# Kernel optimization log

Measured on AMD Instinct MI355X. Metric: run time of the kernel, lower is better.

Reference implementation:

```python
import jax, jax.numpy as jnp
import numpy as np

N = 20000; E = 320000; IN = 128; H = 6; C = 64; HC = H * C; NC = 16; NG = 64


def _gatv2(x, src, dst, wl, bl, wr, br, att, bias, heads, out_c, concat):
    # PyG GATv2Conv (eval mode, share_weights=False, negative_slope=0.2)
    n = x.shape[0]
    xl = (x @ wl + bl).reshape(n, heads, out_c)   # source-side transform
    xr = (x @ wr + br).reshape(n, heads, out_c)   # target-side transform
    # edge-wise attention logits: leaky_relu(x_l[j] + x_r[i]) . att
    e = jnp.einsum('ehc,hc->eh', jax.nn.leaky_relu(xl[src] + xr[dst], 0.2), att)
    # segment softmax over incoming edges of each target node
    emax = jax.ops.segment_max(e, dst, num_segments=n)
    a = jnp.exp(e - emax[dst])
    denom = jax.ops.segment_sum(a, dst, num_segments=n)
    alpha = a / (denom[dst] + 1e-16)
    out = jax.ops.segment_sum(xl[src] * alpha[:, :, None], dst, num_segments=n)
    out = out.reshape(n, heads * out_c) if concat else out.mean(axis=1)
    return out + bias


def setup_inputs() -> dict:
    key = jax.random.key(0)
    ks = jax.random.split(key, 32)
    s = 0.05
    inp = {}
    inp['x'] = jax.random.normal(ks[0], (N, IN), jnp.float32)
    inp['edge_index'] = jax.random.randint(ks[1], (2, E), 0, N, dtype=jnp.int32)
    inp['batch'] = jnp.sort(jax.random.randint(ks[2], (N,), 0, NG, dtype=jnp.int32))
    # input projection (input_dim != hidden_dim * n_heads)
    inp['inp_w'] = jax.random.normal(ks[3], (IN, HC), jnp.float32) * s
    inp['inp_b'] = jnp.zeros((HC,), jnp.float32)
    # layer 0: IN -> (H, C), concat
    inp['l0_wl'] = jax.random.normal(ks[4], (IN, HC), jnp.float32) * s
    inp['l0_bl'] = jnp.zeros((HC,), jnp.float32)
    inp['l0_wr'] = jax.random.normal(ks[5], (IN, HC), jnp.float32) * s
    inp['l0_br'] = jnp.zeros((HC,), jnp.float32)
    inp['l0_att'] = jax.random.normal(ks[6], (H, C), jnp.float32) * s
    inp['l0_bias'] = jnp.zeros((HC,), jnp.float32)
    # layer 1: HC -> (H, C), concat
    inp['l1_wl'] = jax.random.normal(ks[7], (HC, HC), jnp.float32) * s
    inp['l1_bl'] = jnp.zeros((HC,), jnp.float32)
    inp['l1_wr'] = jax.random.normal(ks[8], (HC, HC), jnp.float32) * s
    inp['l1_br'] = jnp.zeros((HC,), jnp.float32)
    inp['l1_att'] = jax.random.normal(ks[9], (H, C), jnp.float32) * s
    inp['l1_bias'] = jnp.zeros((HC,), jnp.float32)
    # layer 2: HC -> (1, C), no concat (mean over the single head)
    inp['l2_wl'] = jax.random.normal(ks[10], (HC, C), jnp.float32) * s
    inp['l2_bl'] = jnp.zeros((C,), jnp.float32)
    inp['l2_wr'] = jax.random.normal(ks[11], (HC, C), jnp.float32) * s
    inp['l2_br'] = jnp.zeros((C,), jnp.float32)
    inp['l2_att'] = jax.random.normal(ks[12], (1, C), jnp.float32) * s
    inp['l2_bias'] = jnp.zeros((C,), jnp.float32)
    # residual projection HC -> C at the last layer (bias-free Linear)
    inp['res_w'] = jax.random.normal(ks[13], (HC, C), jnp.float32) * s
    # dense head: Linear(C,C) + BatchNorm1d(eval) + ReLU + Linear(C,NC)
    inp['d1_w'] = jax.random.normal(ks[14], (C, C), jnp.float32) * s
    inp['d1_b'] = jnp.zeros((C,), jnp.float32)
    inp['bn_g'] = jnp.ones((C,), jnp.float32)
    inp['bn_b'] = jnp.zeros((C,), jnp.float32)
    inp['bn_m'] = jnp.zeros((C,), jnp.float32)
    inp['bn_v'] = jnp.ones((C,), jnp.float32)
    inp['d2_w'] = jax.random.normal(ks[15], (C, NC), jnp.float32) * s
    inp['d2_b'] = jnp.zeros((NC,), jnp.float32)
    return inp


def reference(x, edge_index, batch, inp_w, inp_b,
              l0_wl, l0_bl, l0_wr, l0_br, l0_att, l0_bias,
              l1_wl, l1_bl, l1_wr, l1_br, l1_att, l1_bias,
              l2_wl, l2_bl, l2_wr, l2_br, l2_att, l2_bias,
              res_w, d1_w, d1_b, bn_g, bn_b, bn_m, bn_v, d2_w, d2_b):
    n = x.shape[0]
    sl = jnp.arange(n, dtype=edge_index.dtype)           # self-loops (PyG default)
    src = jnp.concatenate([edge_index[0], sl])
    dst = jnp.concatenate([edge_index[1], sl])
    x_res = x @ inp_w + inp_b
    h = jax.nn.elu(_gatv2(x, src, dst, l0_wl, l0_bl, l0_wr, l0_br, l0_att, l0_bias, H, C, True)) + x_res
    x_res = h
    h = jax.nn.elu(_gatv2(h, src, dst, l1_wl, l1_bl, l1_wr, l1_br, l1_att, l1_bias, H, C, True)) + x_res
    x_res = h
    h = jax.nn.elu(_gatv2(h, src, dst, l2_wl, l2_bl, l2_wr, l2_br, l2_att, l2_bias, 1, C, False)) + x_res @ res_w
    pooled = jax.ops.segment_sum(h, batch, num_segments=NG)
    z = pooled @ d1_w + d1_b
    z = (z - bn_m) / jnp.sqrt(bn_v + 1e-5) * bn_g + bn_b  # BatchNorm1d eval
    z = jax.nn.relu(z) @ d2_w + d2_b
    return h, z
```

## Files before the change

kernel.cpp:

```cpp
#include <hip/hip_runtime.h>
#include <hip/hip_bf16.h>
#include <math.h>

#define NN 20000
#define EE 320000
#define IND 128
#define HH 6
#define CC 64
#define HCC 384
#define NCC 16
#define NGG 64

typedef __bf16 bf16x8 __attribute__((ext_vector_type(8)));
typedef float f32x4 __attribute__((ext_vector_type(4)));
typedef float f32x2 __attribute__((ext_vector_type(2)));
typedef unsigned short ushort_t;
typedef unsigned int uint_t;

#define LOG2E 1.44269504088896f

__device__ inline ushort_t f2bf(float f) {
    union { float f; uint_t u; } x; x.f = f;
    uint_t r = (x.u + 0x7FFF + ((x.u >> 16) & 1)) >> 16;
    return (ushort_t)r;
}
__device__ inline void bf8cvt2(uint4 v, f32x2* f) {
    union { uint_t u; float x; } a, b;
    a.u = v.x << 16; b.u = v.x & 0xFFFF0000u; f[0] = (f32x2){a.x, b.x};
    a.u = v.y << 16; b.u = v.y & 0xFFFF0000u; f[1] = (f32x2){a.x, b.x};
    a.u = v.z << 16; b.u = v.z & 0xFFFF0000u; f[2] = (f32x2){a.x, b.x};
    a.u = v.w << 16; b.u = v.w & 0xFFFF0000u; f[3] = (f32x2){a.x, b.x};
}

template <int CTRL>
__device__ inline float dppadd(float x) {
    int y = __builtin_amdgcn_mov_dpp(__builtin_bit_cast(int, x), CTRL, 0xF, 0xF, true);
    return x + __builtin_bit_cast(float, y);
}

__device__ inline void load_lds16(const ushort_t* g, ushort_t* l) {
    __builtin_amdgcn_global_load_lds(
        (const __attribute__((address_space(1))) void*)g,
        (__attribute__((address_space(3))) void*)l, 16, 0, 0);
}


__global__ void zero_init_kernel(int* counts, int* s6_tail, int* s1_tail, int n) {
    int t = blockIdx.x * blockDim.x + threadIdx.x;
    if (t < n) counts[t] = 0;
    if (t < 8) { s6_tail[t] = 0; s1_tail[t] = 0; }
}

__global__ void count_kernel(const int* __restrict__ ei, int* __restrict__ counts, int E) {
    int t = blockIdx.x * blockDim.x + threadIdx.x;
    if (t < E) atomicAdd(&counts[ei[E + t]], 1);
}

__global__ __launch_bounds__(1024) void scan_kernel(
    const int* __restrict__ counts, int* __restrict__ offsets,
    int* __restrict__ cursor, int n) {
    __shared__ int buf[NN];
    __shared__ int part[1024];
    int t = threadIdx.x;
    for (int idx = t; idx < n; idx += 1024) buf[idx] = counts[idx] + 1;
    __syncthreads();
    int per = (n + 1023) / 1024;
    int base = t * per;
    int sum = 0;
    for (int j = 0; j < per; ++j) {
        int idx = base + j;
        if (idx < n) sum += buf[idx];
    }
    part[t] = sum;
    __syncthreads();
    for (int off = 1; off < 1024; off <<= 1) {
        int v = (t >= off) ? part[t - off] : 0;
        __syncthreads();
        part[t] += v;
        __syncthreads();
    }
    int run = (t == 0) ? 0 : part[t - 1];
    for (int j = 0; j < per; ++j) {
        int idx = base + j;
        if (idx < n) {
            int deg = buf[idx];
            buf[idx] = run;
            run += deg;
        }
    }
    __syncthreads();
    for (int idx = t; idx < n; idx += 1024) {
        int v = buf[idx];
        offsets[idx] = v;
        cursor[idx] = v;
    }
    if (t == 1023) offsets[n] = run;
}

__global__ void fill_kernel(const int* __restrict__ ei, int* __restrict__ cursor,
                            int* __restrict__ srcs6, int* __restrict__ srcs1,
                            int E, int n) {
    int t = blockIdx.x * blockDim.x + threadIdx.x;
    if (t < E) {
        int s = ei[t];
        int d = ei[E + t];
        int slot = atomicAdd(&cursor[d], 1);
        srcs6[slot] = s * 1536;
        srcs1[slot] = s << 8;
    } else if (t < E + n) {
        int i = t - E;
        int slot = atomicAdd(&cursor[i], 1);
        srcs6[slot] = i * 1536;
        srcs1[slot] = i << 8;
    }
}

#define WBIG (1152 * IND)
#define WC1 (768 * HCC)
#define WC2 (192 * HCC)
#define XB_N (NN * IND)
#define PREP_TOTAL (WBIG + WC1 + WC2 + XB_N + 1152 + 768 + 192)

__global__ void prep_kernel(const float* __restrict__ x, const float* __restrict__ inp_w,
    const float* __restrict__ l0wl, const float* __restrict__ l0wr,
    const float* __restrict__ l1wl, const float* __restrict__ l1wr,
    const float* __restrict__ l2wl, const float* __restrict__ l2wr,
    const float* __restrict__ resw,
    const float* __restrict__ inp_b,
    const float* __restrict__ l0bl, const float* __restrict__ l0br,
    const float* __restrict__ l1bl, const float* __restrict__ l1br,
    const float* __restrict__ l2bl, const float* __restrict__ l2br,
    ushort_t* wBig, ushort_t* wC1, ushort_t* wC2, ushort_t* xb,
    float* bBig, float* bC1, float* bC2)
{
    int i = blockIdx.x * blockDim.x + threadIdx.x;
    if (i >= PREP_TOTAL) return;
    if (i < WBIG) {
        int col = i >> 7, k = i & 127;
        float v;
        if (col < 384)      v = inp_w[k * 384 + col];
        else if (col < 768) v = l0wl[k * 384 + (col - 384)];
        else                v = l0wr[k * 384 + (col - 768)];
        wBig[i] = f2bf(v); return;
    }
    i -= WBIG;
    if (i < WC1) {
        int col = i / 384, k = i - col * 384;
        float v = col < 384 ? l1wl[k * 384 + col] : l1wr[k * 384 + (col - 384)];
        wC1[i] = f2bf(v); return;
    }
    i -= WC1;
    if (i < WC2) {
        int col = i / 384, k = i - col * 384;
        float v;
        if (col < 64)       v = resw[k * 64 + col];
        else if (col < 128) v = l2wl[k * 64 + (col - 64)];
        else                v = l2wr[k * 64 + (col - 128)];
        wC2[i] = f2bf(v); return;
    }
    i -= WC2;
    if (i < XB_N) { xb[i] = f2bf(x[i]); return; }
    i -= XB_N;
    if (i < 1152) {
        float v;
        if (i < 384)      v = inp_b[i];
        else if (i < 768) v = l0bl[i - 384];
        else              v = l0br[i - 768];
        bBig[i] = v; return;
    }
    i -= 1152;
    if (i < 768) { bC1[i] = i < 384 ? l1bl[i] : l1br[i - 384]; return; }
    i -= 768;
    if (i < 192) {
        float v;
        if (i < 64)       v = 0.0f;
        else if (i < 128) v = l2bl[i - 64];
        else              v = l2br[i - 128];
        bC2[i] = v; return;
    }
}

__global__ __launch_bounds__(512) void gemm_mfma2(
    const ushort_t* __restrict__ A, const ushort_t* __restrict__ BT,
    const float* __restrict__ bias,
    ushort_t* __restrict__ Cb1, int ld1,
    ushort_t* __restrict__ Cb2, int ld2, int split,
    int M, int N, int K, int NT)
{
    __shared__ ushort_t Bs[2][2][128 * 32];
    int t = threadIdx.x;
    int w = t >> 6, L = t & 63;
    int m0 = blockIdx.x * 256;
    int q = L >> 4, r16 = L & 15;
    int lr = L >> 2;
    int lc = ((L & 3) ^ ((lr >> 1) & 3)) * 8;
    int sw = (q ^ ((r16 >> 1) & 3)) * 8;
    int oB = (w * 16) * 32;

    int rA0 = min(m0 + w * 32 + r16, M - 1);
    int rA1 = min(m0 + w * 32 + 16 + r16, M - 1);
    const ushort_t* pA0base = A + (size_t)rA0 * K + q * 8;
    const ushort_t* pA1base = A + (size_t)rA1 * K + q * 8;

    for (int nt = 0; nt < NT; ++nt) {
        int n0 = (blockIdx.y * NT + nt) * 128;
        int rB = min(n0 + w * 16 + lr, N - 1);
        const ushort_t* gB = BT + (size_t)rB * K + lc;
        const ushort_t* pA0 = pA0base;
        const ushort_t* pA1 = pA1base;

        f32x4 acc[2][8];
#pragma unroll
        for (int a = 0; a < 2; ++a)
#pragma unroll
            for (int b = 0; b < 8; ++b) acc[a][b] = (f32x4){0.f, 0.f, 0.f, 0.f};

        load_lds16(gB, &Bs[0][0][oB]);
        load_lds16(gB + 32, &Bs[0][1][oB]);
        gB += 64;
        bf16x8 a0 = *(const bf16x8*)pA0;
        bf16x8 a2 = *(const bf16x8*)(pA0 + 32);
        bf16x8 a1 = *(const bf16x8*)pA1;
        bf16x8 a3 = *(const bf16x8*)(pA1 + 32);
        pA0 += 64; pA1 += 64;

        int buf = 0;
        for (int k0 = 0; k0 < K; k0 += 64) {
            __syncthreads();
            bool more = (k0 + 64 < K);
            if (more) {
                int nb = buf ^ 1;
                load_lds16(gB, &Bs[nb][0][oB]);
                load_lds16(gB + 32, &Bs[nb][1][oB]);
                gB += 64;
            }
            bf16x8 na0, na1, na2, na3;
            if (more) {
                na0 = *(const bf16x8*)pA0;
                na2 = *(const bf16x8*)(pA0 + 32);
                na1 = *(const bf16x8*)pA1;
                na3 = *(const bf16x8*)(pA1 + 32);
                pA0 += 64; pA1 += 64;
            }
#pragma unroll
            for (int ct = 0; ct < 8; ++ct) {
                bf16x8 blo = *(const bf16x8*)&Bs[buf][0][(ct * 16 + r16) * 32 + sw];
                bf16x8 bhi = *(const bf16x8*)&Bs[buf][1][(ct * 16 + r16) * 32 + sw];
                acc[0][ct] = __builtin_amdgcn_mfma_f32_16x16x32_bf16(blo, a0, acc[0][ct], 0, 0, 0);
                acc[1][ct] = __builtin_amdgcn_mfma_f32_16x16x32_bf16(blo, a1, acc[1][ct], 0, 0, 0);
                acc[0][ct] = __builtin_amdgcn_mfma_f32_16x16x32_bf16(bhi, a2, acc[0][ct], 0, 0, 0);
                acc[1][ct] = __builtin_amdgcn_mfma_f32_16x16x32_bf16(bhi, a3, acc[1][ct], 0, 0, 0);
            }
            if (more) { a0 = na0; a1 = na1; a2 = na2; a3 = na3; }
            buf ^= 1;
        }
#pragma unroll
        for (int rt = 0; rt < 2; ++rt) {
            int row = m0 + w * 32 + rt * 16 + r16;
            if (row >= M) continue;
#pragma unroll
            for (int ct = 0; ct < 8; ++ct) {
                int colb = n0 + ct * 16 + q * 4;
                if (colb >= N) continue;
                float4 bv = *(const float4*)(bias + colb);
                uint2 pk;
                pk.x = (uint_t)f2bf(acc[rt][ct][0] + bv.x) | ((uint_t)f2bf(acc[rt][ct][1] + bv.y) << 16);
                pk.y = (uint_t)f2bf(acc[rt][ct][2] + bv.z) | ((uint_t)f2bf(acc[rt][ct][3] + bv.w) << 16);
                if (colb < split)
                    *(uint2*)(Cb1 + (size_t)row * ld1 + colb) = pk;
                else
                    *(uint2*)(Cb2 + (size_t)row * ld2 + (colb - split)) = pk;
            }
        }
    }
}

__global__ __launch_bounds__(256) void gemm_mfma(
    const ushort_t* __restrict__ A, const ushort_t* __restrict__ BT,
    const float* __restrict__ bias,
    float* __restrict__ Cf, ushort_t* __restrict__ Cb1, int ld1,
    ushort_t* __restrict__ Cb2, int ld2, int split,
    int M, int N, int K)
{
    __shared__ ushort_t Bs[2][2][128 * 32];
    int t = threadIdx.x;
    int w = t >> 6, L = t & 63;
    int m0 = blockIdx.x * 128, n0 = blockIdx.y * 128;
    int q = L >> 4, r16 = L & 15;

    f32x4 acc[2][8];
#pragma unroll
    for (int a = 0; a < 2; ++a)
#pragma unroll
        for (int b = 0; b < 8; ++b) acc[a][b] = (f32x4){0.f, 0.f, 0.f, 0.f};

    int lr = L >> 2;
    int lc = ((L & 3) ^ ((lr >> 1) & 3)) * 8;
    int rB0 = min(n0 + w * 32 + lr, N - 1);
    int rB1 = min(n0 + w * 32 + 16 + lr, N - 1);
    const ushort_t* gB0 = BT + (size_t)rB0 * K + lc;
    const ushort_t* gB1 = BT + (size_t)rB1 * K + lc;
    int oB0 = (w * 32) * 32;
    int oB1 = (w * 32 + 16) * 32;

    int rA0 = min(m0 + w * 32 + r16, M - 1);
    int rA1 = min(m0 + w * 32 + 16 + r16, M - 1);
    const ushort_t* pA0 = A + (size_t)rA0 * K + q * 8;
    const ushort_t* pA1 = A + (size_t)rA1 * K + q * 8;

    int sw = (q ^ ((r16 >> 1) & 3)) * 8;

    load_lds16(gB0, &Bs[0][0][oB0]);
    load_lds16(gB1, &Bs[0][0][oB1]);
    load_lds16(gB0 + 32, &Bs[0][1][oB0]);
    load_lds16(gB1 + 32, &Bs[0][1][oB1]);
    gB0 += 64; gB1 += 64;
    bf16x8 a0 = *(const bf16x8*)pA0;
    bf16x8 a2 = *(const bf16x8*)(pA0 + 32);
    bf16x8 a1 = *(const bf16x8*)pA1;
    bf16x8 a3 = *(const bf16x8*)(pA1 + 32);
    pA0 += 64; pA1 += 64;

    int buf = 0;
    for (int k0 = 0; k0 < K; k0 += 64) {
        __syncthreads();
        bool more = (k0 + 64 < K);
        if (more) {
            int nb = buf ^ 1;
            load_lds16(gB0, &Bs[nb][0][oB0]);
            load_lds16(gB1, &Bs[nb][0][oB1]);
            load_lds16(gB0 + 32, &Bs[nb][1][oB0]);
            load_lds16(gB1 + 32, &Bs[nb][1][oB1]);
            gB0 += 64; gB1 += 64;
        }
        bf16x8 na0, na1, na2, na3;
        if (more) {
            na0 = *(const bf16x8*)pA0;
            na2 = *(const bf16x8*)(pA0 + 32);
            na1 = *(const bf16x8*)pA1;
            na3 = *(const bf16x8*)(pA1 + 32);
            pA0 += 64; pA1 += 64;
        }
#pragma unroll
        for (int ct = 0; ct < 8; ++ct) {
            bf16x8 blo = *(const bf16x8*)&Bs[buf][0][(ct * 16 + r16) * 32 + sw];
            bf16x8 bhi = *(const bf16x8*)&Bs[buf][1][(ct * 16 + r16) * 32 + sw];
            acc[0][ct] = __builtin_amdgcn_mfma_f32_16x16x32_bf16(blo, a0, acc[0][ct], 0, 0, 0);
            acc[1][ct] = __builtin_amdgcn_mfma_f32_16x16x32_bf16(blo, a1, acc[1][ct], 0, 0, 0);
            acc[0][ct] = __builtin_amdgcn_mfma_f32_16x16x32_bf16(bhi, a2, acc[0][ct], 0, 0, 0);
            acc[1][ct] = __builtin_amdgcn_mfma_f32_16x16x32_bf16(bhi, a3, acc[1][ct], 0, 0, 0);
        }
        if (more) { a0 = na0; a1 = na1; a2 = na2; a3 = na3; }
        buf ^= 1;
    }
#pragma unroll
    for (int rt = 0; rt < 2; ++rt) {
        int row = m0 + w * 32 + rt * 16 + r16;
        if (row >= M) continue;
#pragma unroll
        for (int ct = 0; ct < 8; ++ct) {
            int colb = n0 + ct * 16 + q * 4;
            if (colb >= N) continue;
            float4 bv = *(const float4*)(bias + colb);
            float v0 = acc[rt][ct][0] + bv.x;
            float v1 = acc[rt][ct][1] + bv.y;
            float v2 = acc[rt][ct][2] + bv.z;
            float v3 = acc[rt][ct][3] + bv.w;
            if (colb < split) {
                if (Cf) {
                    *(float4*)(Cf + (size_t)row * ld1 + colb) = make_float4(v0, v1, v2, v3);
                } else {
                    uint2 pk;
                    pk.x = (uint_t)f2bf(v0) | ((uint_t)f2bf(v1) << 16);
                    pk.y = (uint_t)f2bf(v2) | ((uint_t)f2bf(v3) << 16);
                    *(uint2*)(Cb1 + (size_t)row * ld1 + colb) = pk;
                }
            } else {
                uint2 pk;
                pk.x = (uint_t)f2bf(v0) | ((uint_t)f2bf(v1) << 16);
                pk.y = (uint_t)f2bf(v2) | ((uint_t)f2bf(v3) << 16);
                *(uint2*)(Cb2 + (size_t)row * ld2 + (colb - split)) = pk;
            }
        }
    }
}

__global__ __launch_bounds__(128) void gat6_kernel(
    const ushort_t* __restrict__ cat, const float* __restrict__ att,
    const float* __restrict__ bias, const ushort_t* __restrict__ resB,
    ushort_t* __restrict__ outB,
    const int* __restrict__ offsets, const int* __restrict__ srcs6, int n)
{
    int wid = (blockIdx.x * blockDim.x + threadIdx.x) >> 6;
    if (wid >= n) return;
    int lane = threadIdx.x & 63;
    int h = lane >> 3, c8 = lane & 7;
    bool hv = h < HH;
    int off = h * 64 + c8 * 8;
    int offL2 = (hv ? off : off - 384) * 2;
    int i = wid;
    int beg = __builtin_amdgcn_readfirstlane(offsets[i]);
    int end = __builtin_amdgcn_readfirstlane(offsets[i + 1]);
    int deg = end - beg;
    int P = (deg + 1) >> 1;
    const char* catc = (const char*)cat;

    f32x2 xr2[4], att2[4];
    {
        uint4 v = *(const uint4*)(catc + (size_t)i * 1536 + 768 + offL2);
        bf8cvt2(v, xr2);
    }
#pragma unroll
    for (int j = 0; j < 4; ++j) {
        int o = (offL2 >> 1) + 2 * j;
        att2[j] = (f32x2){att[o] * LOG2E, att[o + 1] * LOG2E};
    }

    float s = 0.0f;
    f32x2 acc2[4];
#pragma unroll
    for (int j = 0; j < 4; ++j) acc2[j] = (f32x2){0.f, 0.f};

    int bA0 = srcs6[beg], bB0 = srcs6[beg + 1];
    uint4 cA = *(const uint4*)(catc + (size_t)(uint_t)bA0 + offL2);
    uint4 cB = *(const uint4*)(catc + (size_t)(uint_t)bB0 + offL2);
    int iA1 = srcs6[beg + 2], iB1 = srcs6[beg + 3];

    for (int p = 0; p < P; ++p) {
        uint4 nA = cA, nB = cB;
        bool pre = (p + 1 < P);
        if (pre) {
            nA = *(const uint4*)(catc + (size_t)(uint_t)iA1 + offL2);
            nB = *(const uint4*)(catc + (size_t)(uint_t)iB1 + offL2);
            iA1 = srcs6[beg + 2 * p + 4];
            iB1 = srcs6[beg + 2 * p + 5];
        }
        f32x2 xlA[4], xlB[4];
        bf8cvt2(cA, xlA);
        bf8cvt2(cB, xlB);
        f32x2 pA2 = (f32x2){0.f, 0.f}, pB2 = (f32x2){0.f, 0.f};
#pragma unroll
        for (int j = 0; j < 4; ++j) {
            f32x2 ta = xlA[j] + xr2[j];
            ta = __builtin_elementwise_max(ta, ta * 0.2f);
            pA2 += ta * att2[j];
            f32x2 tb = xlB[j] + xr2[j];
            tb = __builtin_elementwise_max(tb, tb * 0.2f);
            pB2 += tb * att2[j];
        }
        float pA = pA2.x + pA2.y, pB = pB2.x + pB2.y;
        pA = dppadd<0xB1>(pA);
        pB = dppadd<0xB1>(pB);
        pA = dppadd<0x4E>(pA);
        pB = dppadd<0x4E>(pB);
        pA = dppadd<0x141>(pA);
        pB = dppadd<0x141>(pB);
        float wA = __builtin_amdgcn_exp2f(pA);
        float wB = (2 * p + 1 < deg) ? __builtin_amdgcn_exp2f(pB) : 0.0f;
        s += wA + wB;
        f32x2 wA2 = (f32x2){wA, wA}, wB2 = (f32x2){wB, wB};
#pragma unroll
        for (int j = 0; j < 4; ++j) {
            acc2[j] += wA2 * xlA[j];
            acc2[j] += wB2 * xlB[j];
        }
        cA = nA; cB = nB;
    }

    if (hv) {
        float inv = 1.0f / (s + 1e-16f);
        size_t ob = (size_t)i * HCC + off;
        uint4 rv = *(const uint4*)(resB + ob);
        f32x2 rr[4];
        bf8cvt2(rv, rr);
        ushort_t u[8];
#pragma unroll
        for (int j = 0; j < 4; ++j) {
            float v0 = acc2[j].x * inv + bias[off + 2 * j];
            float v1 = acc2[j].y * inv + bias[off + 2 * j + 1];
            v0 = v0 > 0.0f ? v0 : expm1f(v0);
            v1 = v1 > 0.0f ? v1 : expm1f(v1);
            u[2 * j]     = f2bf(v0 + rr[j].x);
            u[2 * j + 1] = f2bf(v1 + rr[j].y);
        }
        *(uint4*)(outB + ob) = *(uint4*)u;
    }
}

__global__ __launch_bounds__(128) void gat1_kernel(
    const ushort_t* __restrict__ cat, const float* __restrict__ att,
    const float* __restrict__ bias, const float* __restrict__ res,
    float* __restrict__ out,
    const int* __restrict__ offsets, const int* __restrict__ srcs1, int n)
{
    int wid = (blockIdx.x * blockDim.x + threadIdx.x) >> 6;
    if (wid >= n) return;
    int lane = threadIdx.x & 63;
    int e8 = lane >> 3, c8 = lane & 7;
    int i = wid;
    int beg = __builtin_amdgcn_readfirstlane(offsets[i]);
    int end = __builtin_amdgcn_readfirstlane(offsets[i + 1]);
    const char* catc = (const char*)cat;

    f32x2 xr2[4], att2[4];
    {
        uint4 v = *(const uint4*)(cat + (size_t)i * 128 + 64 + c8 * 8);
        bf8cvt2(v, xr2);
    }
#pragma unroll
    for (int j = 0; j < 4; ++j)
        att2[j] = (f32x2){att[c8 * 8 + 2 * j] * LOG2E, att[c8 * 8 + 2 * j + 1] * LOG2E};

    float s = 0.0f;
    f32x2 acc2[4];
#pragma unroll
    for (int j = 0; j < 4; ++j) acc2[j] = (f32x2){0.f, 0.f};

    const uint4 z = make_uint4(0u, 0u, 0u, 0u);
    int p = beg + e8;
    bool val = p < end;
    int b = val ? srcs1[p] : (i << 8);
    uint4 v = *(const uint4*)(catc + (size_t)(uint_t)b + c8 * 16);

    for (int p0 = beg; p0 < end; p0 += 8) {
        uint4 nv = z;
        bool nval = false;
        if (p0 + 8 < end) {
            int np = p0 + 8 + e8;
            nval = np < end;
            int nb = nval ? srcs1[np] : (i << 8);
            nv = *(const uint4*)(catc + (size_t)(uint_t)nb + c8 * 16);
        }
        f32x2 xl[4];
        bf8cvt2(v, xl);
        f32x2 pp2 = (f32x2){0.f, 0.f};
#pragma unroll
        for (int j = 0; j < 4; ++j) {
            f32x2 tv = xl[j] + xr2[j];
            tv = __builtin_elementwise_max(tv, tv * 0.2f);
            pp2 += tv * att2[j];
        }
        float partial = pp2.x + pp2.y;
        partial = dppadd<0xB1>(partial);
        partial = dppadd<0x4E>(partial);
        partial = dppadd<0x141>(partial);
        float wE = val ? __builtin_amdgcn_exp2f(partial) : 0.0f;
        s += wE;
        f32x2 w2 = (f32x2){wE, wE};
#pragma unroll
        for (int j = 0; j < 4; ++j) acc2[j] += w2 * xl[j];
        v = nv;
        val = nval;
    }

    s = dppadd<0x140>(s);
    s += __shfl_xor(s, 16, 64);
    s += __shfl_xor(s, 32, 64);
#pragma unroll
    for (int j = 0; j < 4; ++j) {
        acc2[j].x += __shfl_xor(acc2[j].x, 8, 64);
        acc2[j].y += __shfl_xor(acc2[j].y, 8, 64);
        acc2[j].x += __shfl_xor(acc2[j].x, 16, 64);
        acc2[j].y += __shfl_xor(acc2[j].y, 16, 64);
        acc2[j].x += __shfl_xor(acc2[j].x, 32, 64);
        acc2[j].y += __shfl_xor(acc2[j].y, 32, 64);
    }
    if (e8 == 0) {
        float inv = 1.0f / (s + 1e-16f);
        size_t ob = (size_t)i * CC + c8 * 8;
        float4 r0 = *(const float4*)(res + ob);
        float4 r1 = *(const float4*)(res + ob + 4);
        float rr[8] = {r0.x, r0.y, r0.z, r0.w, r1.x, r1.y, r1.z, r1.w};
        float av[8] = {acc2[0].x, acc2[0].y, acc2[1].x, acc2[1].y,
                       acc2[2].x, acc2[2].y, acc2[3].x, acc2[3].y};
#pragma unroll
        for (int j = 0; j < 8; ++j) {
            float v2 = av[j] * inv + bias[c8 * 8 + j];
            v2 = v2 > 0.0f ? v2 : expm1f(v2);
            av[j] = v2 + rr[j];
        }
        *(float4*)(out + ob) = make_float4(av[0], av[1], av[2], av[3]);
        *(float4*)(out + ob + 4) = make_float4(av[4], av[5], av[6], av[7]);
    }
}

__global__ __launch_bounds__(256) void pool_kernel(const float* __restrict__ h,
                                                   const int* __restrict__ batch,
                                                   float* __restrict__ pooled, int n) {
    int g = blockIdx.x;
    int t = threadIdx.x;
    int w = t >> 6, lane = t & 63;
    int lo = 0, hi = n;
    while (lo < hi) { int mid = (lo + hi) >> 1; if (batch[mid] < g) lo = mid + 1; else hi = mid; }
    int start = lo;
    int hi2 = n;
    while (lo < hi2) { int mid = (lo + hi2) >> 1; if (batch[mid] < g + 1) lo = mid + 1; else hi2 = mid; }
    int endd = lo;
    float acc = 0.0f;
    for (int r = start + w; r < endd; r += 4)
        acc += h[(size_t)r * 64 + lane];
    __shared__ float red[4][64];
    red[w][lane] = acc;
    __syncthreads();
    if (w == 0)
        pooled[g * 64 + lane] = red[0][lane] + red[1][lane] + red[2][lane] + red[3][lane];
}

__global__ void head_kernel(const float* __restrict__ pooled,
                            const float* __restrict__ d1w, const float* __restrict__ d1b,
                            const float* __restrict__ bng, const float* __restrict__ bnb,
                            const float* __restrict__ bnm, const float* __restrict__ bnv,
                            const float* __restrict__ d2w, const float* __restrict__ d2b,
                            float* __restrict__ zout) {
    __shared__ float z1[64 * 64];
    int t = threadIdx.x;
    for (int idx = t; idx < 64 * 64; idx += 256) {
        int r = idx >> 6, c = idx & 63;
        float acc = d1b[c];
        for (int k = 0; k < 64; ++k) acc += pooled[r * 64 + k] * d1w[k * 64 + c];
        acc = (acc - bnm[c]) / sqrtf(bnv[c] + 1e-5f) * bng[c] + bnb[c];
        z1[idx] = acc > 0.0f ? acc : 0.0f;
    }
    __syncthreads();
    for (int idx = t; idx < 64 * NCC; idx += 256) {
        int r = idx >> 4, c = idx & 15;
        float acc = d2b[c];
        for (int k = 0; k < 64; ++k) acc += z1[r * 64 + k] * d2w[k * NCC + c];
        zout[idx] = acc;
    }
}


extern "C" void kernel_launch(void* const* d_in, const int* in_sizes, int n_in,
                              void* d_out, int out_size, void* d_ws, size_t ws_size,
                              hipStream_t stream) {
    const int N = NN, E = EE, C = CC, HC = HCC, NG = NGG;
    const int EN = E + N;

    const float* x     = (const float*)d_in[0];
    const int*   ei    = (const int*)d_in[1];
    const int*   batch = (const int*)d_in[2];
    const float* inp_w = (const float*)d_in[3];
    const float* inp_b = (const float*)d_in[4];
    const float* l0_wl = (const float*)d_in[5];
    const float* l0_bl = (const float*)d_in[6];
    const float* l0_wr = (const float*)d_in[7];
    const float* l0_br = (const float*)d_in[8];
    const float* l0_att = (const float*)d_in[9];
    const float* l0_bias = (const float*)d_in[10];
    const float* l1_wl = (const float*)d_in[11];
    const float* l1_bl = (const float*)d_in[12];
    const float* l1_wr = (const float*)d_in[13];
    const float* l1_br = (const float*)d_in[14];
    const float* l1_att = (const float*)d_in[15];
    const float* l1_bias = (const float*)d_in[16];
    const float* l2_wl = (const float*)d_in[17];
    const float* l2_bl = (const float*)d_in[18];
    const float* l2_wr = (const float*)d_in[19];
    const float* l2_br = (const float*)d_in[20];
    const float* l2_att = (const float*)d_in[21];
    const float* l2_bias = (const float*)d_in[22];
    const float* res_w = (const float*)d_in[23];
    const float* d1_w = (const float*)d_in[24];
    const float* d1_b = (const float*)d_in[25];
    const float* bn_g = (const float*)d_in[26];
    const float* bn_b = (const float*)d_in[27];
    const float* bn_m = (const float*)d_in[28];
    const float* bn_v = (const float*)d_in[29];
    const float* d2_w = (const float*)d_in[30];
    const float* d2_b = (const float*)d_in[31];

    float* out = (float*)d_out;

    char* ws = (char*)d_ws;
    size_t off = 0;
    auto alloc = [&](size_t bytes) -> void* {
        void* p = ws + off;
        off += (bytes + 255) & ~(size_t)255;
        return p;
    };
    ushort_t* bufH_b  = (ushort_t*)alloc((size_t)N * HC * 2);
    ushort_t* cat01_b = (ushort_t*)alloc((size_t)N * 768 * 2 + 2048);
    ushort_t* xres_b  = (ushort_t*)alloc((size_t)N * HC * 2);
    ushort_t* cat2_b  = (ushort_t*)alloc((size_t)N * 128 * 2);
    float*    bufRes  = (float*)alloc((size_t)N * C * 4);
    ushort_t* xb      = (ushort_t*)alloc((size_t)N * IND * 2);
    ushort_t* wBig    = (ushort_t*)alloc((size_t)WBIG * 2);
    ushort_t* wC1     = (ushort_t*)alloc((size_t)WC1 * 2);
    ushort_t* wC2     = (ushort_t*)alloc((size_t)WC2 * 2);
    float*    bBig    = (float*)alloc((size_t)1152 * 4);
    float*    bC1     = (float*)alloc((size_t)768 * 4);
    float*    bC2     = (float*)alloc((size_t)192 * 4);
    int*      counts  = (int*)alloc((size_t)N * 4);
    int*      cursor  = (int*)alloc((size_t)N * 4);
    int*      offsets = (int*)alloc((size_t)(N + 1) * 4);
    int*      srcs6   = (int*)alloc((size_t)(EN + 8) * 4);
    int*      srcs1   = (int*)alloc((size_t)(EN + 8) * 4);
    float*    pooled  = (float*)alloc((size_t)NG * C * 4);

    zero_init_kernel<<<(N + 255) / 256, 256, 0, stream>>>(counts, srcs6 + EN, srcs1 + EN, N);
    count_kernel<<<(E + 255) / 256, 256, 0, stream>>>(ei, counts, E);
    scan_kernel<<<1, 1024, 0, stream>>>(counts, offsets, cursor, N);
    fill_kernel<<<(EN + 255) / 256, 256, 0, stream>>>(ei, cursor, srcs6, srcs1, E, N);
    prep_kernel<<<(PREP_TOTAL + 255) / 256, 256, 0, stream>>>(
        x, inp_w, l0_wl, l0_wr, l1_wl, l1_wr, l2_wl, l2_wr, res_w,
        inp_b, l0_bl, l0_br, l1_bl, l1_br, l2_bl, l2_br,
        wBig, wC1, wC2, xb, bBig, bC1, bC2);

    int mtiles256 = (N + 255) / 256;
    int mtiles = (N + 127) / 128;
    dim3 gblk(128);
    int gatBlocks = (N * 64 + 127) / 128;

    gemm_mfma2<<<dim3(mtiles256, 3), dim3(512), 0, stream>>>(xb, wBig, bBig,
        xres_b, HC, cat01_b, 768, 384, N, 1152, IND, 3);
    gat6_kernel<<<gatBlocks, gblk, 0, stream>>>(cat01_b, l0_att, l0_bias,
                                                xres_b, bufH_b, offsets, srcs6, N);
    gemm_mfma2<<<dim3(mtiles256, 3), dim3(512), 0, stream>>>(bufH_b, wC1, bC1,
        nullptr, 0, cat01_b, 768, 0, N, 768, HC, 2);
    gat6_kernel<<<gatBlocks, gblk, 0, stream>>>(cat01_b, l1_att, l1_bias,
                                                bufH_b, bufH_b, offsets, srcs6, N);
    gemm_mfma<<<dim3(mtiles, 2), dim3(256), 0, stream>>>(bufH_b, wC2, bC2,
        bufRes, nullptr, C, cat2_b, 128, 64, N, 192, HC);
    gat1_kernel<<<gatBlocks, gblk, 0, stream>>>(cat2_b, l2_att, l2_bias,
                                                bufRes, out, offsets, srcs1, N);
    pool_kernel<<<NG, 256, 0, stream>>>(out, batch, pooled, N);
    head_kernel<<<1, 256, 0, stream>>>(pooled, d1_w, d1_b, bn_g, bn_b, bn_m, bn_v,
                                       d2_w, d2_b, out + (size_t)N * C);
}
```

Before: 428.6 us.

## Fuse CSR build and weight prep into one cooperative kernel

Replaces the five preprocessing kernels (zero, count, single-block scan, fill, prep) with one cooperative kernel that uses grid syncs and a two-level parallel scan across 512 blocks. It also merges the two source-index arrays into one, with gat6 multiplying the index by 6 on load. This is meant to cut launch overhead and the slow single-block scan, and to halve the index writes. The cost is grid-sync latency, and it relies on 512×256 threads covering all NN nodes in the scan (true here).

Measured after the change: 752.7 us. 75.6% more time.

```diff
diff --git a/kernel.cpp b/kernel.cpp
--- a/kernel.cpp
+++ b/kernel.cpp
@@ -1,6 +1,9 @@
 #include <hip/hip_runtime.h>
 #include <hip/hip_bf16.h>
+#include <hip/hip_cooperative_groups.h>
 #include <math.h>
+
+namespace cg = cooperative_groups;
 
 #define NN 20000
 #define EE 320000
@@ -44,84 +47,14 @@
         (__attribute__((address_space(3))) void*)l, 16, 0, 0);
 }
 
-
-__global__ void zero_init_kernel(int* counts, int* s6_tail, int* s1_tail, int n) {
-    int t = blockIdx.x * blockDim.x + threadIdx.x;
-    if (t < n) counts[t] = 0;
-    if (t < 8) { s6_tail[t] = 0; s1_tail[t] = 0; }
-}
-
-__global__ void count_kernel(const int* __restrict__ ei, int* __restrict__ counts, int E) {
-    int t = blockIdx.x * blockDim.x + threadIdx.x;
-    if (t < E) atomicAdd(&counts[ei[E + t]], 1);
-}
-
-__global__ __launch_bounds__(1024) void scan_kernel(
-    const int* __restrict__ counts, int* __restrict__ offsets,
-    int* __restrict__ cursor, int n) {
-    __shared__ int buf[NN];
-    __shared__ int part[1024];
-    int t = threadIdx.x;
-    for (int idx = t; idx < n; idx += 1024) buf[idx] = counts[idx] + 1;
-    __syncthreads();
-    int per = (n + 1023) / 1024;
-    int base = t * per;
-    int sum = 0;
-    for (int j = 0; j < per; ++j) {
-        int idx = base + j;
-        if (idx < n) sum += buf[idx];
-    }
-    part[t] = sum;
-    __syncthreads();
-    for (int off = 1; off < 1024; off <<= 1) {
-        int v = (t >= off) ? part[t - off] : 0;
-        __syncthreads();
-        part[t] += v;
-        __syncthreads();
-    }
-    int run = (t == 0) ? 0 : part[t - 1];
-    for (int j = 0; j < per; ++j) {
-        int idx = base + j;
-        if (idx < n) {
-            int deg = buf[idx];
-            buf[idx] = run;
-            run += deg;
-        }
-    }
-    __syncthreads();
-    for (int idx = t; idx < n; idx += 1024) {
-        int v = buf[idx];
-        offsets[idx] = v;
-        cursor[idx] = v;
-    }
-    if (t == 1023) offsets[n] = run;
-}
-
-__global__ void fill_kernel(const int* __restrict__ ei, int* __restrict__ cursor,
-                            int* __restrict__ srcs6, int* __restrict__ srcs1,
-                            int E, int n) {
-    int t = blockIdx.x * blockDim.x + threadIdx.x;
-    if (t < E) {
-        int s = ei[t];
-        int d = ei[E + t];
-        int slot = atomicAdd(&cursor[d], 1);
-        srcs6[slot] = s * 1536;
-        srcs1[slot] = s << 8;
-    } else if (t < E + n) {
-        int i = t - E;
-        int slot = atomicAdd(&cursor[i], 1);
-        srcs6[slot] = i * 1536;
-        srcs1[slot] = i << 8;
-    }
-}
-
 #define WBIG (1152 * IND)
 #define WC1 (768 * HCC)
 #define WC2 (192 * HCC)
 #define XB_N (NN * IND)
 #define PREP_TOTAL (WBIG + WC1 + WC2 + XB_N + 1152 + 768 + 192)
 
-__global__ void prep_kernel(const float* __restrict__ x, const float* __restrict__ inp_w,
+__device__ inline void prep_elem(int i,
+    const float* __restrict__ x, const float* __restrict__ inp_w,
     const float* __restrict__ l0wl, const float* __restrict__ l0wr,
     const float* __restrict__ l1wl, const float* __restrict__ l1wr,
     const float* __restrict__ l2wl, const float* __restrict__ l2wr,
@@ -133,8 +66,6 @@
     ushort_t* wBig, ushort_t* wC1, ushort_t* wC2, ushort_t* xb,
     float* bBig, float* bC1, float* bC2)
 {
-    int i = blockIdx.x * blockDim.x + threadIdx.x;
-    if (i >= PREP_TOTAL) return;
     if (i < WBIG) {
         int col = i >> 7, k = i & 127;
         float v;
@@ -177,6 +108,87 @@
         else if (i < 128) v = l2bl[i - 64];
         else              v = l2br[i - 128];
         bC2[i] = v; return;
+    }
+}
+
+__global__ __launch_bounds__(256) void pre_kernel(
+    const float* __restrict__ x, const float* __restrict__ inp_w,
+    const float* __restrict__ l0wl, const float* __restrict__ l0wr,
+    const float* __restrict__ l1wl, const float* __restrict__ l1wr,
+    const float* __restrict__ l2wl, const float* __restrict__ l2wr,
+    const float* __restrict__ resw,
+    const float* __restrict__ inp_b,
+    const float* __restrict__ l0bl, const float* __restrict__ l0br,
+    const float* __restrict__ l1bl, const float* __restrict__ l1br,
+    const float* __restrict__ l2bl, const float* __restrict__ l2br,
+    const int* __restrict__ ei,
+    ushort_t* wBig, ushort_t* wC1, ushort_t* wC2, ushort_t* xb,
+    float* bBig, float* bC1, float* bC2,
+    int* counts, int* offsets, int* cursor, int* srcs,
+    int* blockSums, int* blockBase)
+{
+    cg::grid_group g = cg::this_grid();
+    const int TOT = gridDim.x * blockDim.x;
+    int tid = blockIdx.x * blockDim.x + threadIdx.x;
+    int lt = threadIdx.x, bid = blockIdx.x;
+    __shared__ int lp[256];
+
+    for (int i = tid; i < NN; i += TOT) counts[i] = 0;
+    if (tid < 8) srcs[EE + NN + tid] = 0;
+    for (int i = tid; i < PREP_TOTAL; i += TOT)
+        prep_elem(i, x, inp_w, l0wl, l0wr, l1wl, l1wr, l2wl, l2wr, resw,
+                  inp_b, l0bl, l0br, l1bl, l1br, l2bl, l2br,
+                  wBig, wC1, wC2, xb, bBig, bC1, bC2);
+    g.sync();
+
+    for (int t = tid; t < EE; t += TOT) atomicAdd(&counts[ei[EE + t]], 1);
+    g.sync();
+
+    int v = (tid < NN) ? counts[tid] + 1 : 0;
+    lp[lt] = v;
+    __syncthreads();
+    for (int o = 1; o < 256; o <<= 1) {
+        int u = (lt >= o) ? lp[lt - o] : 0;
+        __syncthreads();
+        lp[lt] += u;
+        __syncthreads();
+    }
+    int incl = lp[lt];
+    if (lt == 255) blockSums[bid] = incl;
+    int lexcl = incl - v;
+    g.sync();
+
+    if (bid == 0) {
+        int s0 = blockSums[2 * lt], s1 = blockSums[2 * lt + 1];
+        lp[lt] = s0 + s1;
+        __syncthreads();
+        for (int o = 1; o < 256; o <<= 1) {
+            int u = (lt >= o) ? lp[lt - o] : 0;
+            __syncthreads();
+            lp[lt] += u;
+            __syncthreads();
+        }
+        int pincl = lp[lt];
+        int pexcl = pincl - (s0 + s1);
+        blockBase[2 * lt] = pexcl;
+        blockBase[2 * lt + 1] = pexcl + s0;
+        if (lt == 255) offsets[NN] = pincl;
+    }
+    g.sync();
+
+    if (tid < NN) {
+        int val = blockBase[bid] + lexcl;
+        offsets[tid] = val;
+        cursor[tid] = val;
+    }
+    g.sync();
+
+    for (int t = tid; t < EE + NN; t += TOT) {
+        int s, d;
+        if (t < EE) { s = ei[t]; d = ei[EE + t]; }
+        else        { s = t - EE; d = s; }
+        int slot = atomicAdd(&cursor[d], 1);
+        srcs[slot] = s << 8;
     }
 }
 
@@ -389,7 +401,7 @@
     const ushort_t* __restrict__ cat, const float* __restrict__ att,
     const float* __restrict__ bias, const ushort_t* __restrict__ resB,
     ushort_t* __restrict__ outB,
-    const int* __restrict__ offsets, const int* __restrict__ srcs6, int n)
+    const int* __restrict__ offsets, const int* __restrict__ srcs, int n)
 {
     int wid = (blockIdx.x * blockDim.x + threadIdx.x) >> 6;
     if (wid >= n) return;
@@ -421,10 +433,10 @@
 #pragma unroll
     for (int j = 0; j < 4; ++j) acc2[j] = (f32x2){0.f, 0.f};
 
-    int bA0 = srcs6[beg], bB0 = srcs6[beg + 1];
+    int bA0 = srcs[beg] * 6, bB0 = srcs[beg + 1] * 6;
     uint4 cA = *(const uint4*)(catc + (size_t)(uint_t)bA0 + offL2);
     uint4 cB = *(const uint4*)(catc + (size_t)(uint_t)bB0 + offL2);
-    int iA1 = srcs6[beg + 2], iB1 = srcs6[beg + 3];
+    int iA1 = srcs[beg + 2] * 6, iB1 = srcs[beg + 3] * 6;
 
     for (int p = 0; p < P; ++p) {
         uint4 nA = cA, nB = cB;
@@ -432,8 +444,8 @@
         if (pre) {
             nA = *(const uint4*)(catc + (size_t)(uint_t)iA1 + offL2);
             nB = *(const uint4*)(catc + (size_t)(uint_t)iB1 + offL2);
-            iA1 = srcs6[beg + 2 * p + 4];
-            iB1 = srcs6[beg + 2 * p + 5];
+            iA1 = srcs[beg + 2 * p + 4] * 6;
+            iB1 = srcs[beg + 2 * p + 5] * 6;
         }
         f32x2 xlA[4], xlB[4];
         bf8cvt2(cA, xlA);
@@ -491,7 +503,7 @@
     const ushort_t* __restrict__ cat, const float* __restrict__ att,
     const float* __restrict__ bias, const float* __restrict__ res,
     float* __restrict__ out,
-    const int* __restrict__ offsets, const int* __restrict__ srcs1, int n)
+    const int* __restrict__ offsets, const int* __restrict__ srcs, int n)
 {
     int wid = (blockIdx.x * blockDim.x + threadIdx.x) >> 6;
     if (wid >= n) return;
@@ -519,7 +531,7 @@
     const uint4 z = make_uint4(0u, 0u, 0u, 0u);
     int p = beg + e8;
     bool val = p < end;
-    int b = val ? srcs1[p] : (i << 8);
+    int b = val ? srcs[p] : (i << 8);
     uint4 v = *(const uint4*)(catc + (size_t)(uint_t)b + c8 * 16);
 
     for (int p0 = beg; p0 < end; p0 += 8) {
@@ -528,7 +540,7 @@
         if (p0 + 8 < end) {
             int np = p0 + 8 + e8;
             nval = np < end;
-            int nb = nval ? srcs1[np] : (i << 8);
+            int nb = nval ? srcs[np] : (i << 8);
             nv = *(const uint4*)(catc + (size_t)(uint_t)nb + c8 * 16);
         }
         f32x2 xl[4];
@@ -694,18 +706,31 @@
     int*      counts  = (int*)alloc((size_t)N * 4);
     int*      cursor  = (int*)alloc((size_t)N * 4);
     int*      offsets = (int*)alloc((size_t)(N + 1) * 4);
-    int*      srcs6   = (int*)alloc((size_t)(EN + 8) * 4);
-    int*      srcs1   = (int*)alloc((size_t)(EN + 8) * 4);
+    int*      srcs    = (int*)alloc((size_t)(EN + 8) * 4);
+    int*      blockSums = (int*)alloc((size_t)512 * 4);
+    int*      blockBase = (int*)alloc((size_t)512 * 4);
     float*    pooled  = (float*)alloc((size_t)NG * C * 4);
 
-    zero_init_kernel<<<(N + 255) / 256, 256, 0, stream>>>(counts, srcs6 + EN, srcs1 + EN, N);
-    count_kernel<<<(E + 255) / 256, 256, 0, stream>>>(ei, counts, E);
-    scan_kernel<<<1, 1024, 0, stream>>>(counts, offsets, cursor, N);
-    fill_kernel<<<(EN + 255) / 256, 256, 0, stream>>>(ei, cursor, srcs6, srcs1, E, N);
-    prep_kernel<<<(PREP_TOTAL + 255) / 256, 256, 0, stream>>>(
-        x, inp_w, l0_wl, l0_wr, l1_wl, l1_wr, l2_wl, l2_wr, res_w,
-        inp_b, l0_bl, l0_br, l1_bl, l1_br, l2_bl, l2_br,
-        wBig, wC1, wC2, xb, bBig, bC1, bC2);
+    {
+        void* kp[] = {
+            (void*)&x, (void*)&inp_w,
+            (void*)&l0_wl, (void*)&l0_wr,
+            (void*)&l1_wl, (void*)&l1_wr,
+            (void*)&l2_wl, (void*)&l2_wr,
+            (void*)&res_w,
+            (void*)&inp_b,
+            (void*)&l0_bl, (void*)&l0_br,
+            (void*)&l1_bl, (void*)&l1_br,
+            (void*)&l2_bl, (void*)&l2_br,
+            (void*)&ei,
+            (void*)&wBig, (void*)&wC1, (void*)&wC2, (void*)&xb,
+            (void*)&bBig, (void*)&bC1, (void*)&bC2,
+            (void*)&counts, (void*)&offsets, (void*)&cursor, (void*)&srcs,
+            (void*)&blockSums, (void*)&blockBase
+        };
+        hipLaunchCooperativeKernel((const void*)pre_kernel, dim3(512), dim3(256),
+                                   kp, 0, stream);
+    }
 
     int mtiles256 = (N + 255) / 256;
     int mtiles = (N + 127) / 128;
@@ -715,15 +740,15 @@
     gemm_mfma2<<<dim3(mtiles256, 3), dim3(512), 0, stream>>>(xb, wBig, bBig,
         xres_b, HC, cat01_b, 768, 384, N, 1152, IND, 3);
     gat6_kernel<<<gatBlocks, gblk, 0, stream>>>(cat01_b, l0_att, l0_bias,
-                                                xres_b, bufH_b, offsets, srcs6, N);
+                                                xres_b, bufH_b, offsets, srcs, N);
     gemm_mfma2<<<dim3(mtiles256, 3), dim3(512), 0, stream>>>(bufH_b, wC1, bC1,
         nullptr, 0, cat01_b, 768, 0, N, 768, HC, 2);
     gat6_kernel<<<gatBlocks, gblk, 0, stream>>>(cat01_b, l1_att, l1_bias,
-                                                bufH_b, bufH_b, offsets, srcs6, N);
+                                                bufH_b, bufH_b, offsets, srcs, N);
     gemm_mfma<<<dim3(mtiles, 2), dim3(256), 0, stream>>>(bufH_b, wC2, bC2,
         bufRes, nullptr, C, cat2_b, 128, 64, N, 192, HC);
     gat1_kernel<<<gatBlocks, gblk, 0, stream>>>(cat2_b, l2_att, l2_bias,
-                                                bufRes, out, offsets, srcs1, N);
+                                                bufRes, out, offsets, srcs, N);
     pool_kernel<<<NG, 256, 0, stream>>>(out, batch, pooled, N);
     head_kernel<<<1, 256, 0, stream>>>(pooled, d1_w, d1_b, bn_g, bn_b, bn_m, bn_v,
                                        d2_w, d2_b, out + (size_t)N * C);
```
